# Kernel tuning notes

Measured on AMD Instinct MI355X. Metric: run time of the kernel, lower is better.

The kernel has to match this reference:

```python
import jax, jax.numpy as jnp
import numpy as np

S, E, H, DK, DV, FF = 4096, 1024, 16, 64, 64, 4096
EPS = 1e-5

def setup_inputs() -> dict:
    key = jax.random.key(0)
    ks = jax.random.split(key, 16)
    sc = lambda d: 1.0 / np.sqrt(d)
    return {
        'encoder_input': jax.random.normal(ks[0], (S, E), jnp.float32),
        'Wq': jax.random.normal(ks[1], (E, E), jnp.float32) * sc(E),
        'bq': jnp.zeros((E,), jnp.float32),
        'Wk': jax.random.normal(ks[2], (E, E), jnp.float32) * sc(E),
        'bk': jnp.zeros((E,), jnp.float32),
        'Wv': jax.random.normal(ks[3], (E, E), jnp.float32) * sc(E),
        'bv': jnp.zeros((E,), jnp.float32),
        'Wo': jax.random.normal(ks[4], (E, E), jnp.float32) * sc(E),
        'bo': jnp.zeros((E,), jnp.float32),
        'g1': jnp.ones((E,), jnp.float32),
        'b1': jnp.zeros((E,), jnp.float32),
        'W_ff1': jax.random.normal(ks[5], (E, FF), jnp.float32) * sc(E),
        'b_ff1': jnp.zeros((FF,), jnp.float32),
        'W_ff2': jax.random.normal(ks[6], (FF, E), jnp.float32) * sc(FF),
        'b_ff2': jnp.zeros((E,), jnp.float32),
        'g2': jnp.ones((E,), jnp.float32),
        'b2': jnp.zeros((E,), jnp.float32),
    }

def _layernorm(x, g, b):
    mu = jnp.mean(x, axis=-1, keepdims=True)
    var = jnp.mean(jnp.square(x - mu), axis=-1, keepdims=True)
    return (x - mu) * jax.lax.rsqrt(var + EPS) * g + b

def reference(encoder_input, Wq, bq, Wk, bk, Wv, bv, Wo, bo, g1, b1,
              W_ff1, b_ff1, W_ff2, b_ff2, g2, b2):
    x = encoder_input  # [S, E]
    q = (x @ Wq + bq).reshape(S, H, DK).transpose(1, 0, 2)  # [H,S,dk]
    k = (x @ Wk + bk).reshape(S, H, DK).transpose(1, 0, 2)
    v = (x @ Wv + bv).reshape(S, H, DV).transpose(1, 0, 2)
    scores = jnp.einsum('hqd,hkd->hqk', q, k) / jnp.sqrt(jnp.float32(DK))
    attn = jax.nn.softmax(scores, axis=-1)
    heads = jnp.einsum('hqk,hkd->hqd', attn, v)  # [H,S,dv]
    attn_out = heads.transpose(1, 0, 2).reshape(S, E) @ Wo + bo
    y1 = x + _layernorm(attn_out, g1, b1)
    ff = jax.nn.relu(y1 @ W_ff1 + b_ff1) @ W_ff2 + b_ff2
    return y1 + _layernorm(ff, g2, b2)
```

## Files before the change

kernel.cpp:

```cpp
#include <hip/hip_runtime.h>

typedef unsigned short ushort_t;
typedef unsigned int uint32;
typedef __attribute__((ext_vector_type(8))) __bf16 bf16x8;
typedef __attribute__((ext_vector_type(4))) float f32x4;
typedef __attribute__((ext_vector_type(4))) unsigned short us4;

#define S_LEN 4096
#define EMB   1024
#define NH    16
#define HD    64
#define FFD   4096

__device__ __forceinline__ ushort_t f2b(float f){
  uint32 u = __builtin_bit_cast(uint32, f);
  u += 0x7fffu + ((u >> 16) & 1u);
  return (ushort_t)(u >> 16);
}

__device__ __forceinline__ void gload_lds16(const void* g, void* l){
  __builtin_amdgcn_global_load_lds((const __attribute__((address_space(1))) void*)g,
                                   (__attribute__((address_space(3))) void*)l,
                                   16, 0, 0);
}

__device__ __forceinline__ f32x4 mfma16(bf16x8 a, bf16x8 b, f32x4 c){
  return __builtin_amdgcn_mfma_f32_16x16x32_bf16(a, b, c, 0, 0, 0);
}

template<int EPI>
__global__ __launch_bounds__(256)
void gemm_bt(const ushort_t* __restrict__ A, const ushort_t* __restrict__ BT,
             int M, int N, int K, const float* __restrict__ bias,
             float* __restrict__ outF, ushort_t* __restrict__ outB)
{
  __shared__ __attribute__((aligned(16))) ushort_t As[128 * 32];
  __shared__ __attribute__((aligned(16))) ushort_t Bs[128 * 32];
  const int tid = threadIdx.x;
  const int w = tid >> 6, lane = tid & 63, l16 = lane & 15, lg = lane >> 4;
  const int brow = blockIdx.y * 128, bcol = blockIdx.x * 128;
  const int wr = (w >> 1) * 64, wc = (w & 1) * 64;

  f32x4 acc[4][4];
  #pragma unroll
  for (int m = 0; m < 4; ++m)
    #pragma unroll
    for (int n = 0; n < 4; ++n) acc[m][n] = 0.0f;

  const int r0 = tid >> 2, seg = tid & 3;
  const ushort_t* gA0 = A  + (size_t)(brow + r0) * K      + seg * 8;
  const ushort_t* gA1 = A  + (size_t)(brow + r0 + 64) * K + seg * 8;
  const ushort_t* gB0 = BT + (size_t)(bcol + r0) * K      + seg * 8;
  const ushort_t* gB1 = BT + (size_t)(bcol + r0 + 64) * K + seg * 8;
  ushort_t* lA0 = &As[tid * 8];
  ushort_t* lA1 = &As[(256 + tid) * 8];
  ushort_t* lB0 = &Bs[tid * 8];
  ushort_t* lB1 = &Bs[(256 + tid) * 8];

  const int nk = K >> 5;
  for (int kt = 0; kt < nk; ++kt){
    const int ko = kt * 32;
    gload_lds16(gA0 + ko, lA0);
    gload_lds16(gA1 + ko, lA1);
    gload_lds16(gB0 + ko, lB0);
    gload_lds16(gB1 + ko, lB1);
    __syncthreads();

    bf16x8 af[4], bfr[4];
    #pragma unroll
    for (int m = 0; m < 4; ++m)
      af[m] = *(const bf16x8*)&As[(wr + m * 16 + l16) * 32 + lg * 8];
    #pragma unroll
    for (int n = 0; n < 4; ++n)
      bfr[n] = *(const bf16x8*)&Bs[(wc + n * 16 + l16) * 32 + lg * 8];
    #pragma unroll
    for (int m = 0; m < 4; ++m)
      #pragma unroll
      for (int n = 0; n < 4; ++n)
        acc[m][n] = mfma16(af[m], bfr[n], acc[m][n]);
    __syncthreads();
  }

  #pragma unroll
  for (int n = 0; n < 4; ++n){
    const int col = bcol + wc + n * 16 + l16;
    const float bv = bias[col];
    #pragma unroll
    for (int m = 0; m < 4; ++m){
      const int row0 = brow + wr + m * 16 + lg * 4;
      f32x4 c = acc[m][n];
      #pragma unroll
      for (int r = 0; r < 4; ++r){
        float v = c[r] + bv;
        if (EPI == 2) v = v > 0.f ? v : 0.f;
        if (EPI == 1) outF[(size_t)(row0 + r) * N + col] = v;
        else          outB[(size_t)(row0 + r) * N + col] = f2b(v);
      }
    }
  }
}

__global__ __launch_bounds__(256)
void flash_attn(const ushort_t* __restrict__ qkv, const ushort_t* __restrict__ vt,
                ushort_t* __restrict__ hcat)
{
  __shared__ __attribute__((aligned(16))) ushort_t Ks[2][64 * 64];
  __shared__ __attribute__((aligned(16))) ushort_t Vs[2][64 * 64];
  __shared__ __attribute__((aligned(16))) ushort_t Ps[4][32 * 64];
  const int tid = threadIdx.x, w = tid >> 6, lane = tid & 63;
  const int l16 = lane & 15, lg = lane >> 4, rsw = l16 & 7;
  const int h = blockIdx.y;
  const int q0 = blockIdx.x * 128 + w * 32;

  bf16x8 qf[2][2];
  #pragma unroll
  for (int m = 0; m < 2; ++m)
    #pragma unroll
    for (int kc = 0; kc < 2; ++kc)
      qf[m][kc] = *(const bf16x8*)&qkv[(size_t)(q0 + m * 16 + l16) * 3072 + h * 64 + kc * 32 + lg * 8];

  f32x4 o[2][4];
  float mrun[2][4], lpart[2][4];
  #pragma unroll
  for (int m = 0; m < 2; ++m){
    #pragma unroll
    for (int n = 0; n < 4; ++n) o[m][n] = 0.0f;
    #pragma unroll
    for (int r = 0; r < 4; ++r){ mrun[m][r] = -1e30f; lpart[m][r] = 0.f; }
  }

  const int sr0 = tid >> 3, sc = tid & 7;
  const int sr1 = 32 + sr0;
  const int cc0 = sc ^ (sr0 & 7), cc1 = sc ^ (sr1 & 7);
  const ushort_t* gk0 = qkv + (size_t)sr0 * 3072 + 1024 + h * 64 + cc0 * 8;
  const ushort_t* gk1 = qkv + (size_t)sr1 * 3072 + 1024 + h * 64 + cc1 * 8;
  const ushort_t* gv0 = vt + (size_t)(h * 64 + sr0) * 4096 + cc0 * 8;
  const ushort_t* gv1 = vt + (size_t)(h * 64 + sr1) * 4096 + cc1 * 8;

  auto stage = [&](int buf, int t){
    const int s0 = t * 64;
    gload_lds16(gk0 + (size_t)s0 * 3072, &Ks[buf][tid * 8]);
    gload_lds16(gk1 + (size_t)s0 * 3072, &Ks[buf][(256 + tid) * 8]);
    gload_lds16(gv0 + s0, &Vs[buf][tid * 8]);
    gload_lds16(gv1 + s0, &Vs[buf][(256 + tid) * 8]);
  };
  stage(0, 0);

  const float c2 = 0.18033688011112042f;

  for (int t = 0; t < 64; ++t){
    const int buf = t & 1;
    __syncthreads();
    if (t < 63) stage(buf ^ 1, t + 1);

    f32x4 s[2][4];
    #pragma unroll
    for (int nf = 0; nf < 4; ++nf){
      const int krow = (nf * 16 + l16) * 64;
      bf16x8 kf0 = *(const bf16x8*)&Ks[buf][krow + ((lg     ^ rsw)) * 8];
      bf16x8 kf1 = *(const bf16x8*)&Ks[buf][krow + (((4+lg) ^ rsw)) * 8];
      #pragma unroll
      for (int m = 0; m < 2; ++m){
        f32x4 sv = 0.0f;
        sv = mfma16(qf[m][0], kf0, sv);
        sv = mfma16(qf[m][1], kf1, sv);
        s[m][nf] = sv;
      }
    }

    #pragma unroll
    for (int m = 0; m < 2; ++m){
      float al[4];
      #pragma unroll
      for (int r = 0; r < 4; ++r){
        float vm = fmaxf(fmaxf(s[m][0][r], s[m][1][r]), fmaxf(s[m][2][r], s[m][3][r]));
        vm = fmaxf(vm, __shfl_xor(vm, 1));
        vm = fmaxf(vm, __shfl_xor(vm, 2));
        vm = fmaxf(vm, __shfl_xor(vm, 4));
        vm = fmaxf(vm, __shfl_xor(vm, 8));
        const float mt = vm * c2;
        const float mn = fmaxf(mrun[m][r], mt);
        al[r] = __builtin_amdgcn_exp2f(mrun[m][r] - mn);
        mrun[m][r] = mn;
      }
      #pragma unroll
      for (int nf = 0; nf < 4; ++nf)
        #pragma unroll
        for (int r = 0; r < 4; ++r)
          s[m][nf][r] = __builtin_amdgcn_exp2f(__builtin_fmaf(s[m][nf][r], c2, -mrun[m][r]));
      #pragma unroll
      for (int r = 0; r < 4; ++r){
        const float su = (s[m][0][r] + s[m][1][r]) + (s[m][2][r] + s[m][3][r]);
        lpart[m][r] = lpart[m][r] * al[r] + su;
      }
      #pragma unroll
      for (int n = 0; n < 4; ++n)
        #pragma unroll
        for (int r = 0; r < 4; ++r) o[m][n][r] *= al[r];
      #pragma unroll
      for (int r = 0; r < 4; ++r){
        const int q = m * 16 + lg * 4 + r;
        const int swz = (q & 7) << 4;
        char* base = (char*)&Ps[w][0] + q * 128;
        #pragma unroll
        for (int nf = 0; nf < 4; ++nf){
          const int kvb = (nf * 16 + l16) * 2;
          *(ushort_t*)(base + (kvb ^ swz)) = f2b(s[m][nf][r]);
        }
      }
    }
    asm volatile("s_waitcnt lgkmcnt(0)" ::: "memory");
    __builtin_amdgcn_sched_barrier(0);

    #pragma unroll
    for (int kvc = 0; kvc < 2; ++kvc){
      bf16x8 pf[2];
      #pragma unroll
      for (int m = 0; m < 2; ++m){
        const int row = m * 16 + l16;
        const int off = (kvc * 64 + lg * 16) ^ ((row & 7) << 4);
        pf[m] = *(const bf16x8*)((const char*)&Ps[w][0] + row * 128 + off);
      }
      #pragma unroll
      for (int n = 0; n < 4; ++n){
        bf16x8 vf = *(const bf16x8*)&Vs[buf][(n * 16 + l16) * 64 + (((kvc * 4 + lg) ^ rsw)) * 8];
        #pragma unroll
        for (int m = 0; m < 2; ++m) o[m][n] = mfma16(pf[m], vf, o[m][n]);
      }
    }
  }

  #pragma unroll
  for (int m = 0; m < 2; ++m){
    float linv[4];
    #pragma unroll
    for (int r = 0; r < 4; ++r){
      float l = lpart[m][r];
      l += __shfl_xor(l, 1); l += __shfl_xor(l, 2);
      l += __shfl_xor(l, 4); l += __shfl_xor(l, 8);
      linv[r] = 1.f / l;
    }
    #pragma unroll
    for (int n = 0; n < 4; ++n)
      #pragma unroll
      for (int r = 0; r < 4; ++r){
        const size_t row = q0 + m * 16 + lg * 4 + r;
        hcat[row * 1024 + h * 64 + n * 16 + l16] = f2b(o[m][n][r] * linv[r]);
      }
  }
}

template<bool WB>
__global__ __launch_bounds__(256)
void ln_res(const float* __restrict__ in, const float* __restrict__ res,
            const float* __restrict__ g, const float* __restrict__ b,
            float* __restrict__ outF, ushort_t* __restrict__ outB)
{
  const int row = blockIdx.x, tid = threadIdx.x, w = tid >> 6, lane = tid & 63;
  const float4 v = ((const float4*)(in + (size_t)row * 1024))[tid];
  float s  = v.x + v.y + v.z + v.w;
  float s2 = v.x * v.x + v.y * v.y + v.z * v.z + v.w * v.w;
  #pragma unroll
  for (int off = 1; off < 64; off <<= 1){
    s  += __shfl_xor(s, off);
    s2 += __shfl_xor(s2, off);
  }
  __shared__ float red[8];
  if (lane == 0){ red[w] = s; red[4 + w] = s2; }
  __syncthreads();
  s  = red[0] + red[1] + red[2] + red[3];
  s2 = red[4] + red[5] + red[6] + red[7];
  const float mu   = s  * (1.f / 1024.f);
  const float var  = s2 * (1.f / 1024.f) - mu * mu;
  const float rstd = rsqrtf(var + 1e-5f);
  const float4 gv = ((const float4*)g)[tid];
  const float4 bv = ((const float4*)b)[tid];
  const float4 rv = ((const float4*)(res + (size_t)row * 1024))[tid];
  float4 y;
  y.x = rv.x + (v.x - mu) * rstd * gv.x + bv.x;
  y.y = rv.y + (v.y - mu) * rstd * gv.y + bv.y;
  y.z = rv.z + (v.z - mu) * rstd * gv.z + bv.z;
  y.w = rv.w + (v.w - mu) * rstd * gv.w + bv.w;
  ((float4*)(outF + (size_t)row * 1024))[tid] = y;
  if (WB){
    us4 u; u.x = f2b(y.x); u.y = f2b(y.y); u.z = f2b(y.z); u.w = f2b(y.w);
    ((us4*)(outB + (size_t)row * 1024))[tid] = u;
  }
}

__global__ void transpose_f2b(const float* __restrict__ in, int ldin,
                              ushort_t* __restrict__ out, int ldout)
{
  __shared__ float tile[32][33];
  const int bx = blockIdx.x * 32, by = blockIdx.y * 32;
  const int tx = threadIdx.x, ty = threadIdx.y;
  #pragma unroll
  for (int i = 0; i < 32; i += 8)
    tile[ty + i][tx] = in[(size_t)(by + ty + i) * ldin + bx + tx];
  __syncthreads();
  #pragma unroll
  for (int i = 0; i < 32; i += 8)
    out[(size_t)(bx + ty + i) * ldout + by + tx] = f2b(tile[tx][ty + i]);
}

__global__ void transpose_b2b(const ushort_t* __restrict__ in, int ldin,
                              ushort_t* __restrict__ out, int ldout)
{
  __shared__ ushort_t tile[32][34];
  const int bx = blockIdx.x * 32, by = blockIdx.y * 32;
  const int tx = threadIdx.x, ty = threadIdx.y;
  #pragma unroll
  for (int i = 0; i < 32; i += 8)
    tile[ty + i][tx] = in[(size_t)(by + ty + i) * ldin + bx + tx];
  __syncthreads();
  #pragma unroll
  for (int i = 0; i < 32; i += 8)
    out[(size_t)(bx + ty + i) * ldout + by + tx] = tile[tx][ty + i];
}

__global__ void cast_f2b_k(const float* __restrict__ in, ushort_t* __restrict__ out, int n4)
{
  for (int i = blockIdx.x * blockDim.x + threadIdx.x; i < n4; i += gridDim.x * blockDim.x){
    const float4 v = ((const float4*)in)[i];
    us4 u; u.x = f2b(v.x); u.y = f2b(v.y); u.z = f2b(v.z); u.w = f2b(v.w);
    ((us4*)out)[i] = u;
  }
}

__global__ void concat3(const float* __restrict__ a, const float* __restrict__ b,
                        const float* __restrict__ c, float* __restrict__ out)
{
  const int i = blockIdx.x * 256 + threadIdx.x;
  out[i] = i < 1024 ? a[i] : (i < 2048 ? b[i - 1024] : c[i - 2048]);
}

extern "C" void kernel_launch(void* const* d_in, const int* in_sizes, int n_in,
                              void* d_out, int out_size, void* d_ws, size_t ws_size,
                              hipStream_t stream)
{
  (void)in_sizes; (void)n_in; (void)out_size; (void)ws_size;
  const float* x   = (const float*)d_in[0];
  const float* Wq  = (const float*)d_in[1];
  const float* bq  = (const float*)d_in[2];
  const float* Wk  = (const float*)d_in[3];
  const float* bk  = (const float*)d_in[4];
  const float* Wv  = (const float*)d_in[5];
  const float* bv  = (const float*)d_in[6];
  const float* Wo  = (const float*)d_in[7];
  const float* bo  = (const float*)d_in[8];
  const float* g1  = (const float*)d_in[9];
  const float* b1  = (const float*)d_in[10];
  const float* Wf1 = (const float*)d_in[11];
  const float* bf1 = (const float*)d_in[12];
  const float* Wf2 = (const float*)d_in[13];
  const float* bf2 = (const float*)d_in[14];
  const float* g2  = (const float*)d_in[15];
  const float* b2  = (const float*)d_in[16];
  float* out = (float*)d_out;

  char* p = (char*)d_ws;
  auto alloc = [&](size_t bytes){ char* r = p; p += (bytes + 255) & ~(size_t)255; return r; };
  ushort_t* xb    = (ushort_t*)alloc((size_t)S_LEN * EMB * 2);
  ushort_t* wqkvT = (ushort_t*)alloc((size_t)3072 * 1024 * 2);
  ushort_t* wOT   = (ushort_t*)alloc((size_t)1024 * 1024 * 2);
  ushort_t* wf1T  = (ushort_t*)alloc((size_t)4096 * 1024 * 2);
  ushort_t* wf2T  = (ushort_t*)alloc((size_t)1024 * 4096 * 2);
  float*    bqkv  = (float*)alloc(3072 * 4);
  ushort_t* qkv   = (ushort_t*)alloc((size_t)4096 * 3072 * 2);
  ushort_t* vtb   = (ushort_t*)alloc((size_t)1024 * 4096 * 2);
  ushort_t* hcat  = (ushort_t*)alloc((size_t)4096 * 1024 * 2);
  float*    attnO = (float*)alloc((size_t)4096 * 1024 * 4);
  float*    y1    = (float*)alloc((size_t)4096 * 1024 * 4);
  ushort_t* y1b   = (ushort_t*)alloc((size_t)4096 * 1024 * 2);
  ushort_t* ff1 = qkv;
  float*    ff2 = attnO;

  const dim3 tb(32, 8);
  cast_f2b_k<<<2048, 256, 0, stream>>>(x, xb, S_LEN * EMB / 4);
  transpose_f2b<<<dim3(32, 32),  tb, 0, stream>>>(Wq, 1024, wqkvT,                 1024);
  transpose_f2b<<<dim3(32, 32),  tb, 0, stream>>>(Wk, 1024, wqkvT + 1024 * 1024,   1024);
  transpose_f2b<<<dim3(32, 32),  tb, 0, stream>>>(Wv, 1024, wqkvT + 2048 * 1024,   1024);
  transpose_f2b<<<dim3(32, 32),  tb, 0, stream>>>(Wo, 1024, wOT,  1024);
  transpose_f2b<<<dim3(128, 32), tb, 0, stream>>>(Wf1, 4096, wf1T, 1024);
  transpose_f2b<<<dim3(32, 128), tb, 0, stream>>>(Wf2, 1024, wf2T, 4096);
  concat3<<<12, 256, 0, stream>>>(bq, bk, bv, bqkv);

  gemm_bt<0><<<dim3(3072 / 128, 4096 / 128), 256, 0, stream>>>(
      xb, wqkvT, 4096, 3072, 1024, bqkv, nullptr, qkv);
  transpose_b2b<<<dim3(32, 128), tb, 0, stream>>>(qkv + 2048, 3072, vtb, 4096);
  flash_attn<<<dim3(32, 16), 256, 0, stream>>>(qkv, vtb, hcat);
  gemm_bt<1><<<dim3(1024 / 128, 4096 / 128), 256, 0, stream>>>(
      hcat, wOT, 4096, 1024, 1024, bo, attnO, nullptr);
  ln_res<true><<<4096, 256, 0, stream>>>(attnO, x, g1, b1, y1, y1b);
  gemm_bt<2><<<dim3(4096 / 128, 4096 / 128), 256, 0, stream>>>(
      y1b, wf1T, 4096, 4096, 1024, bf1, nullptr, ff1);
  gemm_bt<1><<<dim3(1024 / 128, 4096 / 128), 256, 0, stream>>>(
      ff1, wf2T, 4096, 1024, 4096, bf2, ff2, nullptr);
  ln_res<false><<<4096, 256, 0, stream>>>(ff2, y1, g2, b2, out, nullptr);
}
```

Before: 575.7 us.

## Compute transposed S in flash attention to keep P in registers

The attention kernel now computes S^T (K as the A operand, Q as B), so each lane holds the probabilities for one query column and can feed them straight into the PV MFMA without the LDS round-trip through Ps. K rows are loaded in a permuted order so the register layout matches the MFMA A-operand. Each wave now handles 16 queries instead of 32, the grid doubles, and launch bounds request 4 blocks per CU. A lazy rescale skips the O correction unless the running max grows by more than 8 (log2 units). This trades half the K/V reuse per block for less LDS traffic and higher occupancy, and the lazy rescale relies on bounded exponent growth for accuracy.

```diff
diff --git a/kernel.cpp b/kernel.cpp
--- a/kernel.cpp
+++ b/kernel.cpp
@@ -26,6 +26,11 @@
 
 __device__ __forceinline__ f32x4 mfma16(bf16x8 a, bf16x8 b, f32x4 c){
   return __builtin_amdgcn_mfma_f32_16x16x32_bf16(a, b, c, 0, 0, 0);
+}
+
+__device__ __forceinline__ float bperm_f(int srclane, float v){
+  return __builtin_bit_cast(float,
+      __builtin_amdgcn_ds_bpermute(srclane * 4, __builtin_bit_cast(int, v)));
 }
 
 template<int EPI>
@@ -100,47 +105,41 @@
   }
 }
 
-__global__ __launch_bounds__(256)
+__global__ __launch_bounds__(256, 4)
 void flash_attn(const ushort_t* __restrict__ qkv, const ushort_t* __restrict__ vt,
                 ushort_t* __restrict__ hcat)
 {
   __shared__ __attribute__((aligned(16))) ushort_t Ks[2][64 * 64];
   __shared__ __attribute__((aligned(16))) ushort_t Vs[2][64 * 64];
-  __shared__ __attribute__((aligned(16))) ushort_t Ps[4][32 * 64];
   const int tid = threadIdx.x, w = tid >> 6, lane = tid & 63;
   const int l16 = lane & 15, lg = lane >> 4, rsw = l16 & 7;
   const int h = blockIdx.y;
-  const int q0 = blockIdx.x * 128 + w * 32;
-
-  bf16x8 qf[2][2];
-  #pragma unroll
-  for (int m = 0; m < 2; ++m)
-    #pragma unroll
-    for (int kc = 0; kc < 2; ++kc)
-      qf[m][kc] = *(const bf16x8*)&qkv[(size_t)(q0 + m * 16 + l16) * 3072 + h * 64 + kc * 32 + lg * 8];
-
-  f32x4 o[2][4];
-  float mrun[2][4], lpart[2][4];
-  #pragma unroll
-  for (int m = 0; m < 2; ++m){
-    #pragma unroll
-    for (int n = 0; n < 4; ++n) o[m][n] = 0.0f;
-    #pragma unroll
-    for (int r = 0; r < 4; ++r){ mrun[m][r] = -1e30f; lpart[m][r] = 0.f; }
-  }
+  const int q0 = blockIdx.x * 64 + w * 16;
+
+  bf16x8 qf[2];
+  #pragma unroll
+  for (int kc = 0; kc < 2; ++kc)
+    qf[kc] = *(const bf16x8*)&qkv[(size_t)(q0 + l16) * 3072 + h * 64 + kc * 32 + lg * 8];
+
+  f32x4 o[4];
+  #pragma unroll
+  for (int n = 0; n < 4; ++n) o[n] = 0.0f;
+  float mrun = -1e30f, lpart = 0.f;
 
   const int sr0 = tid >> 3, sc = tid & 7;
   const int sr1 = 32 + sr0;
   const int cc0 = sc ^ (sr0 & 7), cc1 = sc ^ (sr1 & 7);
-  const ushort_t* gk0 = qkv + (size_t)sr0 * 3072 + 1024 + h * 64 + cc0 * 8;
-  const ushort_t* gk1 = qkv + (size_t)sr1 * 3072 + 1024 + h * 64 + cc1 * 8;
+  const int pr0 = ((sr0 >> 2) & 3) * 8 + ((sr0 >> 4) & 1) * 4 + (sr0 & 3) + ((sr0 >> 5) & 1) * 32;
+  const int pr1 = ((sr1 >> 2) & 3) * 8 + ((sr1 >> 4) & 1) * 4 + (sr1 & 3) + ((sr1 >> 5) & 1) * 32;
+  const ushort_t* gk0 = qkv + (size_t)pr0 * 3072 + 1024 + h * 64 + cc0 * 8;
+  const ushort_t* gk1 = qkv + (size_t)pr1 * 3072 + 1024 + h * 64 + cc1 * 8;
   const ushort_t* gv0 = vt + (size_t)(h * 64 + sr0) * 4096 + cc0 * 8;
   const ushort_t* gv1 = vt + (size_t)(h * 64 + sr1) * 4096 + cc1 * 8;
 
   auto stage = [&](int buf, int t){
-    const int s0 = t * 64;
-    gload_lds16(gk0 + (size_t)s0 * 3072, &Ks[buf][tid * 8]);
-    gload_lds16(gk1 + (size_t)s0 * 3072, &Ks[buf][(256 + tid) * 8]);
+    const size_t s0 = (size_t)t * 64;
+    gload_lds16(gk0 + s0 * 3072, &Ks[buf][tid * 8]);
+    gload_lds16(gk1 + s0 * 3072, &Ks[buf][(256 + tid) * 8]);
     gload_lds16(gv0 + s0, &Vs[buf][tid * 8]);
     gload_lds16(gv1 + s0, &Vs[buf][(256 + tid) * 8]);
   };
@@ -153,101 +152,83 @@
     __syncthreads();
     if (t < 63) stage(buf ^ 1, t + 1);
 
-    f32x4 s[2][4];
+    f32x4 s[4];
     #pragma unroll
     for (int nf = 0; nf < 4; ++nf){
       const int krow = (nf * 16 + l16) * 64;
       bf16x8 kf0 = *(const bf16x8*)&Ks[buf][krow + ((lg     ^ rsw)) * 8];
       bf16x8 kf1 = *(const bf16x8*)&Ks[buf][krow + (((4+lg) ^ rsw)) * 8];
-      #pragma unroll
-      for (int m = 0; m < 2; ++m){
-        f32x4 sv = 0.0f;
-        sv = mfma16(qf[m][0], kf0, sv);
-        sv = mfma16(qf[m][1], kf1, sv);
-        s[m][nf] = sv;
-      }
+      f32x4 sv = 0.0f;
+      sv = mfma16(kf0, qf[0], sv);
+      sv = mfma16(kf1, qf[1], sv);
+      s[nf] = sv;
     }
 
-    #pragma unroll
-    for (int m = 0; m < 2; ++m){
-      float al[4];
-      #pragma unroll
-      for (int r = 0; r < 4; ++r){
-        float vm = fmaxf(fmaxf(s[m][0][r], s[m][1][r]), fmaxf(s[m][2][r], s[m][3][r]));
-        vm = fmaxf(vm, __shfl_xor(vm, 1));
-        vm = fmaxf(vm, __shfl_xor(vm, 2));
-        vm = fmaxf(vm, __shfl_xor(vm, 4));
-        vm = fmaxf(vm, __shfl_xor(vm, 8));
-        const float mt = vm * c2;
-        const float mn = fmaxf(mrun[m][r], mt);
-        al[r] = __builtin_amdgcn_exp2f(mrun[m][r] - mn);
-        mrun[m][r] = mn;
-      }
-      #pragma unroll
-      for (int nf = 0; nf < 4; ++nf)
-        #pragma unroll
-        for (int r = 0; r < 4; ++r)
-          s[m][nf][r] = __builtin_amdgcn_exp2f(__builtin_fmaf(s[m][nf][r], c2, -mrun[m][r]));
-      #pragma unroll
-      for (int r = 0; r < 4; ++r){
-        const float su = (s[m][0][r] + s[m][1][r]) + (s[m][2][r] + s[m][3][r]);
-        lpart[m][r] = lpart[m][r] * al[r] + su;
-      }
+    float vm = s[0][0];
+    #pragma unroll
+    for (int nf = 0; nf < 4; ++nf)
+      #pragma unroll
+      for (int r = 0; r < 4; ++r) vm = fmaxf(vm, s[nf][r]);
+    vm = fmaxf(vm, __shfl_xor(vm, 16));
+    vm = fmaxf(vm, __shfl_xor(vm, 32));
+    const float ms = vm * c2;
+
+    if (__any(ms > mrun + 8.f)){
+      const float mn = fmaxf(mrun, ms);
+      const float al = __builtin_amdgcn_exp2f(mrun - mn);
+      mrun = mn;
+      lpart *= al;
+      float alo[4];
+      #pragma unroll
+      for (int r = 0; r < 4; ++r) alo[r] = bperm_f(lg * 4 + r, al);
       #pragma unroll
       for (int n = 0; n < 4; ++n)
         #pragma unroll
-        for (int r = 0; r < 4; ++r) o[m][n][r] *= al[r];
+        for (int r = 0; r < 4; ++r) o[n][r] *= alo[r];
+    }
+
+    float lsum = 0.f;
+    #pragma unroll
+    for (int nf = 0; nf < 4; ++nf)
       #pragma unroll
       for (int r = 0; r < 4; ++r){
-        const int q = m * 16 + lg * 4 + r;
-        const int swz = (q & 7) << 4;
-        char* base = (char*)&Ps[w][0] + q * 128;
-        #pragma unroll
-        for (int nf = 0; nf < 4; ++nf){
-          const int kvb = (nf * 16 + l16) * 2;
-          *(ushort_t*)(base + (kvb ^ swz)) = f2b(s[m][nf][r]);
-        }
+        const float p = __builtin_amdgcn_exp2f(__builtin_fmaf(s[nf][r], c2, -mrun));
+        s[nf][r] = p;
+        lsum += p;
       }
-    }
-    asm volatile("s_waitcnt lgkmcnt(0)" ::: "memory");
-    __builtin_amdgcn_sched_barrier(0);
-
-    #pragma unroll
-    for (int kvc = 0; kvc < 2; ++kvc){
-      bf16x8 pf[2];
-      #pragma unroll
-      for (int m = 0; m < 2; ++m){
-        const int row = m * 16 + l16;
-        const int off = (kvc * 64 + lg * 16) ^ ((row & 7) << 4);
-        pf[m] = *(const bf16x8*)((const char*)&Ps[w][0] + row * 128 + off);
-      }
+    lpart += lsum;
+
+    bf16x8 pa[2];
+    #pragma unroll
+    for (int nf = 0; nf < 4; ++nf)
+      #pragma unroll
+      for (int r = 0; r < 4; ++r)
+        pa[nf >> 1][(nf & 1) * 4 + r] = (__bf16)s[nf][r];
+
+    #pragma unroll
+    for (int kvc = 0; kvc < 2; ++kvc)
       #pragma unroll
       for (int n = 0; n < 4; ++n){
         bf16x8 vf = *(const bf16x8*)&Vs[buf][(n * 16 + l16) * 64 + (((kvc * 4 + lg) ^ rsw)) * 8];
-        #pragma unroll
-        for (int m = 0; m < 2; ++m) o[m][n] = mfma16(pf[m], vf, o[m][n]);
+        o[n] = mfma16(pa[kvc], vf, o[n]);
       }
+  }
+
+  float lt = lpart;
+  lt += __shfl_xor(lt, 16);
+  lt += __shfl_xor(lt, 32);
+  const float linv = 1.f / lt;
+  float linvo[4];
+  #pragma unroll
+  for (int r = 0; r < 4; ++r) linvo[r] = bperm_f(lg * 4 + r, linv);
+
+  #pragma unroll
+  for (int n = 0; n < 4; ++n)
+    #pragma unroll
+    for (int r = 0; r < 4; ++r){
+      const size_t row = q0 + lg * 4 + r;
+      hcat[row * 1024 + h * 64 + n * 16 + l16] = f2b(o[n][r] * linvo[r]);
     }
-  }
-
-  #pragma unroll
-  for (int m = 0; m < 2; ++m){
-    float linv[4];
-    #pragma unroll
-    for (int r = 0; r < 4; ++r){
-      float l = lpart[m][r];
-      l += __shfl_xor(l, 1); l += __shfl_xor(l, 2);
-      l += __shfl_xor(l, 4); l += __shfl_xor(l, 8);
-      linv[r] = 1.f / l;
-    }
-    #pragma unroll
-    for (int n = 0; n < 4; ++n)
-      #pragma unroll
-      for (int r = 0; r < 4; ++r){
-        const size_t row = q0 + m * 16 + lg * 4 + r;
-        hcat[row * 1024 + h * 64 + n * 16 + l16] = f2b(o[m][n][r] * linv[r]);
-      }
-  }
 }
 
 template<bool WB>
@@ -388,7 +369,7 @@
   gemm_bt<0><<<dim3(3072 / 128, 4096 / 128), 256, 0, stream>>>(
       xb, wqkvT, 4096, 3072, 1024, bqkv, nullptr, qkv);
   transpose_b2b<<<dim3(32, 128), tb, 0, stream>>>(qkv + 2048, 3072, vtb, 4096);
-  flash_attn<<<dim3(32, 16), 256, 0, stream>>>(qkv, vtb, hcat);
+  flash_attn<<<dim3(64, 16), 256, 0, stream>>>(qkv, vtb, hcat);
   gemm_bt<1><<<dim3(1024 / 128, 4096 / 128), 256, 0, stream>>>(
       hcat, wOT, 4096, 1024, 1024, bo, attnO, nullptr);
   ln_res<true><<<4096, 256, 0, stream>>>(attnO, x, g1, b1, y1, y1b);
```

Measured after the change: 481.7 us. 16.3% less time.
